# Kernel optimization log

Hardware: AMD Instinct MI355X
Metric: run time of the kernel (lower is better)

The kernel has to match this reference:

```python
import jax, jax.numpy as jnp
import numpy as np

B, N, IN_DIM, D, H = 8, 2048, 256, 512, 4
HD = D // H
GX, GY = 8, 8
IMG_W, IMG_H = 256.0, 256.0
CW, CH = IMG_W / GX, IMG_H / GY
NBH = 1
EPS = 1e-5


def setup_inputs() -> dict:
    key = jax.random.key(0)
    ks = jax.random.split(key, 12)
    s = 0.02
    rn = lambda k, sh: jax.random.normal(k, sh, jnp.float32) * s
    return {
        'features': jax.random.normal(ks[0], (B, N, IN_DIM), jnp.float32),
        'coords': jax.random.uniform(ks[1], (B, N, 2), jnp.float32) * IMG_W,
        'W_feat': rn(ks[2], (IN_DIM, D)), 'b_feat': jnp.zeros((D,), jnp.float32),
        'W_p1': rn(ks[3], (2, D // 2)), 'b_p1': jnp.zeros((D // 2,), jnp.float32),
        'W_p2': rn(ks[4], (D // 2, D)), 'b_p2': jnp.zeros((D,), jnp.float32),
        'Wq': rn(ks[5], (D, D)), 'bq': jnp.zeros((D,), jnp.float32),
        'Wk': rn(ks[6], (D, D)), 'bk': jnp.zeros((D,), jnp.float32),
        'Wv': rn(ks[7], (D, D)), 'bv': jnp.zeros((D,), jnp.float32),
        'Wo': rn(ks[8], (D, D)), 'bo': jnp.zeros((D,), jnp.float32),
        'gamma': jnp.ones((D,), jnp.float32), 'beta': jnp.zeros((D,), jnp.float32),
    }


def reference(features, coords, W_feat, b_feat, W_p1, b_p1, W_p2, b_p2,
              Wq, bq, Wk, bk, Wv, bv, Wo, bo, gamma, beta):
    feat = features @ W_feat + b_feat                          # [B,N,D]
    # --- grid bucketing (mean feature per occupied cell) ---
    gx = jnp.clip((coords[..., 0] / CW).astype(jnp.int32), 0, GX - 1)
    gy = jnp.clip((coords[..., 1] / CH).astype(jnp.int32), 0, GY - 1)
    cell = gx * GY + gy                                        # [B,N]
    G = GX * GY
    seg = (jnp.arange(B, dtype=jnp.int32)[:, None] * G + cell).reshape(-1)
    sums = jax.ops.segment_sum(feat.reshape(B * N, D), seg, num_segments=B * G)
    counts = jax.ops.segment_sum(jnp.ones((B * N,), jnp.float32), seg, num_segments=B * G)
    mean = (sums / jnp.maximum(counts, 1.0)[:, None]).reshape(B, G, D)
    counts = counts.reshape(B, G)
    # --- neighbor cells (static 3x3 window for neighborhood=1) ---
    offs = np.array([(dx, dy) for dx in range(-NBH, NBH + 1) for dy in range(-NBH, NBH + 1)], np.int32)
    K = offs.shape[0]
    pe = jnp.asarray(offs, jnp.float32)
    pe = jax.nn.relu(pe @ W_p1 + b_p1) @ W_p2 + b_p2           # [K,D] pos enc of offsets
    ngx = gx[..., None] + offs[:, 0]                           # [B,N,K]
    ngy = gy[..., None] + offs[:, 1]
    inb = (ngx >= 0) & (ngx < GX) & (ngy >= 0) & (ngy < GY)
    nidx = jnp.clip(ngx, 0, GX - 1) * GY + jnp.clip(ngy, 0, GY - 1)
    bidx = jnp.arange(B)[:, None, None]
    valid = inb & (counts[bidx, nidx] > 0)                     # [B,N,K]
    keys = mean[bidx, nidx] + pe                               # [B,N,K,D]
    # --- per-point attention over <=9 neighbor cells ---
    q = (feat @ Wq + bq).reshape(B, N, H, HD)
    k = (keys @ Wk + bk).reshape(B, N, K, H, HD)
    v = (keys @ Wv + bv).reshape(B, N, K, H, HD)
    scores = jnp.einsum('bnhd,bnkhd->bnhk', q, k) / np.float32(np.sqrt(HD))
    scores = jnp.where(valid[:, :, None, :], scores, jnp.float32(-1e9))
    attn = jax.nn.softmax(scores, axis=-1)
    agg = jnp.einsum('bnhk,bnkhd->bnhd', attn, v).reshape(B, N, D) @ Wo + bo
    enhanced = feat + agg                                      # residual (dropout in eval = identity)
    mu = enhanced.mean(-1, keepdims=True)
    var = enhanced.var(-1, keepdims=True)
    return (enhanced - mu) / jnp.sqrt(var + EPS) * gamma + beta
```

## Files before the change

### kernel.cpp

```cpp
#include <hip/hip_runtime.h>
#include <stdint.h>

typedef unsigned short u16;
typedef unsigned int u32;
typedef __bf16 bf16x8 __attribute__((ext_vector_type(8)));
typedef float f32x4 __attribute__((ext_vector_type(4)));

#define NBATCH 8
#define NPT    2048
#define NPTS   16384
#define INDIM  256
#define DD     512
#define GG     64

__device__ __forceinline__ u16 f2bf(float f){
  u32 u = __builtin_bit_cast(u32, f);
  u += 0x7fffu + ((u >> 16) & 1u);
  return (u16)(u >> 16);
}
__device__ __forceinline__ float bf2f(u16 h){
  u32 u = ((u32)h) << 16;
  return __builtin_bit_cast(float, u);
}
__device__ __forceinline__ void load8(const float* __restrict__ p, float* r){
  float4 a = *(const float4*)p;
  float4 b = *(const float4*)(p + 4);
  r[0]=a.x;r[1]=a.y;r[2]=a.z;r[3]=a.w;r[4]=b.x;r[5]=b.y;r[6]=b.z;r[7]=b.w;
}
__device__ __forceinline__ void load8bf(const u16* __restrict__ p, float* r){
  uint4 v = *(const uint4*)p;
  r[0]=bf2f((u16)v.x); r[1]=bf2f((u16)(v.x>>16));
  r[2]=bf2f((u16)v.y); r[3]=bf2f((u16)(v.y>>16));
  r[4]=bf2f((u16)v.z); r[5]=bf2f((u16)(v.z>>16));
  r[6]=bf2f((u16)v.w); r[7]=bf2f((u16)(v.w>>16));
}
__device__ __forceinline__ void load8bf_lds(const u16* p, float* r){
  uint4 v = *(const uint4*)p;
  r[0]=bf2f((u16)v.x); r[1]=bf2f((u16)(v.x>>16));
  r[2]=bf2f((u16)v.y); r[3]=bf2f((u16)(v.y>>16));
  r[4]=bf2f((u16)v.z); r[5]=bf2f((u16)(v.z>>16));
  r[6]=bf2f((u16)v.w); r[7]=bf2f((u16)(v.w>>16));
}
__device__ __forceinline__ void store8(float* __restrict__ p, const float* r){
  float4 a; a.x=r[0];a.y=r[1];a.z=r[2];a.w=r[3];
  float4 b; b.x=r[4];b.y=r[5];b.z=r[6];b.w=r[7];
  *(float4*)p = a; *(float4*)(p+4) = b;
}
__device__ __forceinline__ uint4 pack8(const float* a){
  uint4 pk;
  pk.x = (u32)f2bf(a[0]) | ((u32)f2bf(a[1]) << 16);
  pk.y = (u32)f2bf(a[2]) | ((u32)f2bf(a[3]) << 16);
  pk.z = (u32)f2bf(a[4]) | ((u32)f2bf(a[5]) << 16);
  pk.w = (u32)f2bf(a[6]) | ((u32)f2bf(a[7]) << 16);
  return pk;
}
typedef __attribute__((address_space(1))) unsigned as1u;
typedef __attribute__((address_space(3))) unsigned as3u;
__device__ __forceinline__ void gload16(const void* g, void* l){
  __builtin_amdgcn_global_load_lds((as1u*)(uintptr_t)g, (as3u*)(uintptr_t)l, 16, 0, 0);
}

__device__ __forceinline__ void transpose64(const float* __restrict__ src, int scols,
                                            u16* __restrict__ dst, int dcols,
                                            int r0, int c0, char* smem, int t){
  float (*sh)[65] = (float(*)[65])smem;
  #pragma unroll
  for (int i = 0; i < 16; i++){
    int idx = i*256 + t;
    int r = idx >> 6, c = idx & 63;
    sh[r][c] = src[(size_t)(r0 + r)*scols + c0 + c];
  }
  __syncthreads();
  #pragma unroll
  for (int i = 0; i < 8; i++){
    int idx = i*512 + t*2;
    int oR = idx >> 6, oC = idx & 63;
    u32 pk = (u32)f2bf(sh[oC][oR]) | ((u32)f2bf(sh[oC+1][oR]) << 16);
    *(u32*)(dst + (size_t)(c0 + oR)*dcols + r0 + oC) = pk;
  }
}

#define P_R1 2048
#define P_R2 2112
#define P_R3 2368
#define P_R4 2400
#define P_R5 2409
#define P_R6 2411
#define P_R7 2415
#define P_NB 2423
__global__ __launch_bounds__(256) void prep_kernel(
    const float* __restrict__ features, const float* __restrict__ W_feat,
    const float* __restrict__ Wq, const float* __restrict__ Wk,
    const float* __restrict__ Wv, const float* __restrict__ Wo,
    const float* __restrict__ W_p1, const float* __restrict__ b_p1,
    const float* __restrict__ W_p2, const float* __restrict__ b_p2,
    const float* __restrict__ b_feat, const float* __restrict__ bq,
    const float* __restrict__ bk, const float* __restrict__ bv,
    const float* __restrict__ coords,
    u16* __restrict__ featA, u16* __restrict__ W_feat_bf,
    u16* __restrict__ WqkvT, u16* __restrict__ WoT, u16* __restrict__ WcatT,
    u16* __restrict__ peD, float* __restrict__ bfq, float* __restrict__ biaskv,
    int* __restrict__ order, int* __restrict__ counts, int* __restrict__ cellstart)
{
  __shared__ __align__(16) char smem[34048];
  int bid = blockIdx.x, t = threadIdx.x;
  if (bid < P_R1){
    int i = bid*256 + t;
    float r[8]; load8(features + (size_t)i*8, r);
    *(uint4*)(featA + (size_t)i*8) = pack8(r);
  } else if (bid < P_R2){
    int i = (bid - P_R1)*256 + t;
    float r[8]; load8(W_feat + (size_t)i*8, r);
    *(uint4*)(W_feat_bf + (size_t)i*8) = pack8(r);
  } else if (bid < P_R3){
    int rel = bid - P_R2;
    int mat = rel >> 6, tile = rel & 63;
    int r0 = (tile >> 3)*64, c0 = (tile & 7)*64;
    const float* src = mat==0 ? Wq : (mat==1 ? Wk : (mat==2 ? Wv : Wo));
    u16* dst = mat==0 ? WqkvT : (mat==1 ? WqkvT + (size_t)512*DD
                     : (mat==2 ? WqkvT + (size_t)1024*DD : WoT));
    transpose64(src, DD, dst, DD, r0, c0, smem, t);
  } else if (bid < P_R4){
    int rel = bid - P_R3;
    int r0 = (rel >> 3)*64, c0 = (rel & 7)*64;
    transpose64(W_feat, DD, WcatT, INDIM, r0, c0, smem, t);
  } else if (bid < P_R5){
    int kk = bid - P_R4;
    float dx = (float)(kk/3 - 1), dy = (float)(kk%3 - 1);
    float* h = (float*)smem;
    float hv = dx*W_p1[t] + dy*W_p1[256 + t] + b_p1[t];
    h[t] = hv > 0.f ? hv : 0.f;
    __syncthreads();
    float acc0 = b_p2[t], acc1 = b_p2[t + 256];
    for (int c = 0; c < 256; c++){
      float hc = h[c];
      acc0 += hc * W_p2[(size_t)c*DD + t];
      acc1 += hc * W_p2[(size_t)c*DD + t + 256];
    }
    peD[(size_t)kk*DD + t]       = f2bf(acc0);
    peD[(size_t)kk*DD + t + 256] = f2bf(acc1);
  } else if (bid < P_R6){
    int i = (bid - P_R5)*256 + t;
    float* bfs = (float*)smem;
    bfs[t] = b_feat[t]; bfs[t + 256] = b_feat[t + 256];
    __syncthreads();
    float acc = 0.f;
    for (int k = 0; k < DD; k++) acc += bfs[k] * Wq[(size_t)k*DD + i];
    bfq[i] = acc + bq[i];
  } else if (bid < P_R7){
    int n = (bid - P_R6)*256 + t;
    float* bfs = (float*)smem;
    bfs[t] = b_feat[t]; bfs[t + 256] = b_feat[t + 256];
    __syncthreads();
    const float* W = (n < 512) ? Wk : Wv;
    int c = n & 511;
    float acc = 0.f;
    for (int k = 0; k < DD; k++) acc += bfs[k] * W[(size_t)k*DD + c];
    biaskv[n] = acc + ((n < 512) ? bk[c] : bv[c]);
  } else {
    int b = bid - P_R7;
    u16 (*hist)[65] = (u16(*)[65])smem;
    int* tot  = (int*)(smem + 33280);
    int* base = (int*)(smem + 33536);
    #pragma unroll
    for (int i = 0; i < 65; i++) hist[t][i] = 0;
    int myc[8];
    float cxy[16];
    load8(coords + (size_t)(b*NPT + t*8)*2,     cxy);
    load8(coords + (size_t)(b*NPT + t*8)*2 + 8, cxy + 8);
    #pragma unroll
    for (int i = 0; i < 8; i++){
      int gx = (int)(cxy[2*i]   * (1.0f/32.0f)); gx = gx < 0 ? 0 : (gx > 7 ? 7 : gx);
      int gy = (int)(cxy[2*i+1] * (1.0f/32.0f)); gy = gy < 0 ? 0 : (gy > 7 ? 7 : gy);
      myc[i] = gx*8 + gy;
      hist[t][myc[i]]++;
    }
    __syncthreads();
    if (t < GG){
      int acc = 0;
      for (int tt = 0; tt < 256; tt++){ int v = hist[tt][t]; hist[tt][t] = (u16)acc; acc += v; }
      tot[t] = acc;
    }
    __syncthreads();
    if (t == 0){
      int acc = 0;
      for (int g = 0; g < GG; g++){ base[g] = acc; acc += tot[g]; }
    }
    __syncthreads();
    if (t < GG){
      counts[b*GG + t] = tot[t];
      cellstart[b*GG + t] = base[t];
    }
    #pragma unroll
    for (int i = 0; i < 8; i++){
      int g = myc[i];
      int local = 0;
      #pragma unroll
      for (int j = 0; j < 8; j++) local += (j < i && myc[j] == g) ? 1 : 0;
      order[b*NPT + base[g] + (int)hist[t][g] + local] = t*8 + i;
    }
  }
}

#define BM 128
#define BN 128
#define GEMM_PIPE(SMEMB, Aptr, Btptr, Kv, GXv, NWGv, UIDX)                         \
  u16* lA_ = (u16*)(SMEMB);                                                        \
  u16* lB_ = (u16*)((char*)(SMEMB) + 16384);                                       \
  int orig_ = (UIDX);                                                              \
  int swz_ = (orig_ & 7)*((NWGv) >> 3) + (orig_ >> 3);                             \
  int m0 = (swz_ / (GXv)) * BM, n0 = (swz_ % (GXv)) * BN;                          \
  int lane = tid & 63;                                                             \
  int wv = tid >> 6;                                                               \
  int wm = (wv >> 1) * 64, wn = (wv & 1) * 64;                                     \
  int lr = lane & 15;                                                              \
  int kg = (lane >> 4) << 3;                                                       \
  f32x4 acc[4][4] = {};                                                            \
  {                                                                                \
    int srow = lane >> 2;                                                          \
    int scol = (lane & 3) << 3;                                                    \
    const u16* gA0 = (Aptr)  + (size_t)(m0 + wv*32 + srow)*(Kv) + scol;            \
    const u16* gB0 = (Btptr) + (size_t)(n0 + wv*32 + srow)*(Kv) + scol;            \
    int lofs = (wv*32)*32;                                                         \
    int steps = (Kv) >> 5;                                                         \
    gload16(gA0,                   lA_ + lofs);                                    \
    gload16(gA0 + (size_t)16*(Kv), lA_ + lofs + 512);                              \
    gload16(gB0,                   lB_ + lofs);                                    \
    gload16(gB0 + (size_t)16*(Kv), lB_ + lofs + 512);                              \
    __syncthreads();                                                               \
    for (int s = 0; s < steps; s++){                                               \
      int cur = s & 1;                                                             \
      u16* lAc = lA_ + cur*4096;                                                   \
      u16* lBc = lB_ + cur*4096;                                                   \
      if (s + 1 < steps){                                                          \
        int kt = (s + 1) << 5;                                                     \
        u16* lAn = lA_ + (cur^1)*4096;                                             \
        u16* lBn = lB_ + (cur^1)*4096;                                             \
        gload16(gA0 + kt,                   lAn + lofs);                           \
        gload16(gA0 + kt + (size_t)16*(Kv), lAn + lofs + 512);                     \
        gload16(gB0 + kt,                   lBn + lofs);                           \
        gload16(gB0 + kt + (size_t)16*(Kv), lBn + lofs + 512);                     \
      }                                                                            \
      bf16x8 af[4], bfv[4];                                                        \
      _Pragma("unroll")                                                            \
      for (int i = 0; i < 4; i++) af[i]  = *(const bf16x8*)&lAc[(wm + i*16 + lr)*32 + kg]; \
      _Pragma("unroll")                                                            \
      for (int j = 0; j < 4; j++) bfv[j] = *(const bf16x8*)&lBc[(wn + j*16 + lr)*32 + kg]; \
      _Pragma("unroll")                                                            \
      for (int i = 0; i < 4; i++)                                                  \
        _Pragma("unroll")                                                          \
        for (int j = 0; j < 4; j++)                                                \
          acc[i][j] = __builtin_amdgcn_mfma_f32_16x16x32_bf16(af[i], bfv[j], acc[i][j], 0, 0, 0); \
      __syncthreads();                                                             \
    }                                                                              \
  }                                                                                \
  int lrow = (lane >> 4) << 2;

#define EPI_BF16(SMEMB, DST, LDN, BIAS)                                            \
  {                                                                                \
    u16* Cs = (u16*)(SMEMB);                                                       \
    _Pragma("unroll")                                                              \
    for (int j = 0; j < 4; j++){                                                   \
      int col = wn + j*16 + lr;                                                    \
      float bcol = (BIAS)[n0 + col];                                               \
      _Pragma("unroll")                                                            \
      for (int i = 0; i < 4; i++){                                                 \
        int r0 = wm + i*16 + lrow;                                                 \
        _Pragma("unroll")                                                          \
        for (int r = 0; r < 4; r++)                                                \
          Cs[(r0 + r)*136 + col] = f2bf(acc[i][j][r] + bcol);                      \
      }                                                                            \
    }                                                                              \
    __syncthreads();                                                               \
    _Pragma("unroll")                                                              \
    for (int k = 0; k < 8; k++){                                                   \
      int idx = k*256 + tid;                                                       \
      int row = idx >> 4, c8 = (idx & 15) << 3;                                    \
      *(uint4*)&(DST)[(size_t)(m0 + row)*(LDN) + n0 + c8] = *(uint4*)&Cs[row*136 + c8]; \
    }                                                                              \
  }

__global__ __launch_bounds__(256) void mid_kernel(
    const u16* __restrict__ WqkvT, const u16* __restrict__ W_feat_bf,
    const u16* __restrict__ peD, u16* __restrict__ Xout, float* __restrict__ meanKV,
    const u16* __restrict__ featA, const int* __restrict__ order,
    const int* __restrict__ counts, const int* __restrict__ cellstart,
    u16* __restrict__ meanF, const u16* __restrict__ WcatT,
    const float* __restrict__ b_feat, u16* __restrict__ feat_bf)
{
  __shared__ __align__(16) char SMEM[34816];
  int tid = threadIdx.x;
  if (blockIdx.x < 24){
    GEMM_PIPE(SMEM, WqkvT, W_feat_bf, 512, 2, 24, (int)blockIdx.x)
    #pragma unroll
    for (int j = 0; j < 4; j++){
      int col = n0 + wn + j*16 + lr;
      #pragma unroll
      for (int i = 0; i < 4; i++){
        int row0 = m0 + wm + i*16 + lrow;
        #pragma unroll
        for (int r = 0; r < 4; r++)
          Xout[(size_t)(row0 + r)*INDIM + col] = f2bf(acc[i][j][r]);
      }
    }
  } else if (blockIdx.x < 60){
    float* pesh = (float*)SMEM;
    int bid2 = blockIdx.x - 24;
    int kk = bid2 >> 2, seg = bid2 & 3;
    int n = seg*256 + tid;
    pesh[tid]       = bf2f(peD[(size_t)kk*DD + tid]);
    pesh[tid + 256] = bf2f(peD[(size_t)kk*DD + tid + 256]);
    __syncthreads();
    const u16* wrow = WqkvT + (size_t)(512 + n)*DD;
    float acc = 0.f;
    for (int d8 = 0; d8 < 64; d8++){
      float w8[8]; load8bf(wrow + d8*8, w8);
      #pragma unroll
      for (int j = 0; j < 8; j++) acc += pesh[d8*8 + j]*w8[j];
    }
    meanKV[(size_t)(512 + kk)*1024 + n] = acc;
  } else if (blockIdx.x < 572){
    float (*part)[2] = (float(*)[2])SMEM;
    int bg = blockIdx.x - 60;
    int b = bg >> 6;
    int p = tid & 127, half = tid >> 7;
    int cnt = counts[bg], start = cellstart[bg];
    const int* ord = order + b*NPT + start;
    float a0 = 0.f, a1 = 0.f;
    for (int n = half; n < cnt; n += 2){
      u32 v = *(const u32*)(featA + (((size_t)(b*NPT + ord[n])) << 8) + p*2);
      a0 += bf2f((u16)v); a1 += bf2f((u16)(v >> 16));
    }
    if (half){ part[p][0] = a0; part[p][1] = a1; }
    __syncthreads();
    if (!half){
      a0 += part[p][0]; a1 += part[p][1];
      float inv = 1.f / (float)(cnt > 0 ? cnt : 1);
      *(u32*)(meanF + (size_t)bg*INDIM + p*2) =
          (u32)f2bf(a0*inv) | ((u32)f2bf(a1*inv) << 16);
    }
  } else {
    GEMM_PIPE(SMEM, featA, WcatT, 256, 4, 512, (int)blockIdx.x - 572)
    EPI_BF16(SMEM, feat_bf, DD, b_feat)
  }
}

__global__ __launch_bounds__(256) void qmean_kernel(
    const u16* __restrict__ featA, const u16* __restrict__ WfqT,
    const u16* __restrict__ meanF, const u16* __restrict__ WfkvT,
    const float* __restrict__ bfq, const float* __restrict__ biaskv,
    u16* __restrict__ q_bf, float* __restrict__ meanKV)
{
  __shared__ __align__(16) char SMEM[34816];
  int tid = threadIdx.x;
  if (blockIdx.x < 512){
    GEMM_PIPE(SMEM, featA, WfqT, 256, 4, 512, (int)blockIdx.x)
    EPI_BF16(SMEM, q_bf, DD, bfq)
  } else {
    GEMM_PIPE(SMEM, meanF, WfkvT, 256, 8, 32, (int)blockIdx.x - 512)
    #pragma unroll
    for (int j = 0; j < 4; j++){
      int col = n0 + wn + j*16 + lr;
      float bcol = biaskv[col];
      #pragma unroll
      for (int i = 0; i < 4; i++){
        int row0 = m0 + wm + i*16 + lrow;
        #pragma unroll
        for (int r = 0; r < 4; r++)
          meanKV[(size_t)(row0 + r)*1024 + col] = acc[i][j][r] + bcol;
      }
    }
  }
}

__global__ __launch_bounds__(1024) void attn_cells(
    const u16* __restrict__ q, const float* __restrict__ meanKV,
    const int* __restrict__ order, const int* __restrict__ counts,
    const int* __restrict__ cellstart, u16* __restrict__ agg)
{
  int bg = blockIdx.x;
  int b = bg >> 6, c = bg & 63;
  int gx = c >> 3, gy = c & 7;
  __shared__ __align__(16) u16 Kf[9][DD];
  __shared__ __align__(16) u16 Vf[9][DD];
  __shared__ int vrow[9];
  int t = threadIdx.x;
  if (t < 9){
    int dx = t/3 - 1, dy = t%3 - 1;
    int nx = gx + dx, ny = gy + dy;
    int inb = ((unsigned)nx < 8u) && ((unsigned)ny < 8u);
    int row = b*GG + (((nx&7) << 3) | (ny&7));
    vrow[t] = (inb && counts[row] > 0) ? row : -1;
  }
  __syncthreads();
  int d = 2*(t & 255);
  for (int kk = (t >> 8); kk < 9; kk += 4){
    int row = vrow[kk];
    if (row >= 0){
      float2 mk = *(const float2*)&meanKV[(size_t)row*1024 + d];
      float2 pk = *(const float2*)&meanKV[(size_t)(512+kk)*1024 + d];
      float2 mv = *(const float2*)&meanKV[(size_t)row*1024 + 512 + d];
      float2 pv = *(const float2*)&meanKV[(size_t)(512+kk)*1024 + 512 + d];
      *(u32*)&Kf[kk][d] = (u32)f2bf(mk.x+pk.x) | ((u32)f2bf(mk.y+pk.y) << 16);
      *(u32*)&Vf[kk][d] = (u32)f2bf(mv.x+pv.x) | ((u32)f2bf(mv.y+pv.y) << 16);
    }
  }
  __syncthreads();
  int cnt = counts[bg];
  int wv = t >> 6, lane = t & 63;
  const int* ord = order + b*NPT + cellstart[bg];
  for (int i = wv; i < cnt; i += 16){
    size_t p = (size_t)b*NPT + ord[i];
    float qv[8];
    load8bf(q + p*DD + lane*8, qv);
    float s[9];
    #pragma unroll
    for (int kk = 0; kk < 9; kk++){
      float partial = 0.f;
      if (vrow[kk] >= 0){
        float kv[8]; load8bf(&Kf[kk][lane*8], kv);
        #pragma unroll
        for (int j = 0; j < 8; j++) partial += qv[j]*kv[j];
      }
      partial += __shfl_xor(partial, 1);
      partial += __shfl_xor(partial, 2);
      partial += __shfl_xor(partial, 4);
      partial += __shfl_xor(partial, 8);
      s[kk] = (vrow[kk] >= 0) ? partial * 0.08838834764831843f : -1e30f;
    }
    float mx = s[0];
    #pragma unroll
    for (int kk = 1; kk < 9; kk++) mx = fmaxf(mx, s[kk]);
    float w[9], sum = 0.f;
    #pragma unroll
    for (int kk = 0; kk < 9; kk++){
      w[kk] = (vrow[kk] >= 0) ? __expf(s[kk] - mx) : 0.f;
      sum += w[kk];
    }
    float inv = 1.f / sum;
    float a[8] = {0,0,0,0,0,0,0,0};
    #pragma unroll
    for (int kk = 0; kk < 9; kk++){
      if (vrow[kk] >= 0){
        float wk = w[kk] * inv;
        float vv[8]; load8bf(&Vf[kk][lane*8], vv);
        #pragma unroll
        for (int j = 0; j < 8; j++) a[j] += wk*vv[j];
      }
    }
    *(uint4*)&agg[p*DD + lane*8] = pack8(a);
  }
}

__global__ __launch_bounds__(512) void linln_kernel(
    const u16* __restrict__ agg_bf, const u16* __restrict__ WoT,
    const float* __restrict__ bo, const u16* __restrict__ feat_bf,
    const float* __restrict__ gamma, const float* __restrict__ beta,
    float* __restrict__ out)
{
  __shared__ __align__(16) char SMEM[73728];
  u16* lA = (u16*)SMEM;
  u16* lB = (u16*)(SMEM + 8192);
  int tid = threadIdx.x;
  int lane = tid & 63;
  int wvv = tid >> 6;
  int m0 = blockIdx.x * 64;
  int wm2 = (wvv >> 2) * 32;
  int wn2 = (wvv & 3) * 128;
  int lr = lane & 15;
  int kg = (lane >> 4) << 3;
  int srow = lane >> 2;
  int scol = (lane & 3) << 3;
  f32x4 acc[2][8] = {};
  {
    const u16* gB0 = WoT + (size_t)(wvv*64 + srow)*DD + scol;
    int lBoff = (wvv*64)*32;
    const u16* gA0 = agg_bf + (size_t)(m0 + (wvv&3)*16 + srow)*DD + scol;
    int lAoff = ((wvv&3)*16)*32;
    bool doA = (wvv < 4);
    #pragma unroll
    for (int c = 0; c < 4; c++)
      gload16(gB0 + (size_t)(c*16)*DD, lB + lBoff + c*16*32);
    if (doA) gload16(gA0, lA + lAoff);
    __syncthreads();
    for (int s = 0; s < 16; s++){
      int cur = s & 1;
      u16* lAc = lA + cur*2048;
      u16* lBc = lB + cur*16384;
      if (s + 1 < 16){
        int kt = (s + 1) << 5;
        u16* lAn = lA + (cur^1)*2048;
        u16* lBn = lB + (cur^1)*16384;
        #pragma unroll
        for (int c = 0; c < 4; c++)
          gload16(gB0 + kt + (size_t)(c*16)*DD, lBn + lBoff + c*16*32);
        if (doA) gload16(gA0 + kt, lAn + lAoff);
      }
      bf16x8 af[2], bfv[8];
      #pragma unroll
      for (int i = 0; i < 2; i++) af[i]  = *(const bf16x8*)&lAc[(wm2 + i*16 + lr)*32 + kg];
      #pragma unroll
      for (int j = 0; j < 8; j++) bfv[j] = *(const bf16x8*)&lBc[(wn2 + j*16 + lr)*32 + kg];
      #pragma unroll
      for (int i = 0; i < 2; i++)
        #pragma unroll
        for (int j = 0; j < 8; j++)
          acc[i][j] = __builtin_amdgcn_mfma_f32_16x16x32_bf16(af[i], bfv[j], acc[i][j], 0, 0, 0);
      __syncthreads();
    }
  }
  int lrow = (lane >> 4) << 2;
  u16* Cs = (u16*)SMEM;
  #pragma unroll
  for (int j = 0; j < 8; j++){
    int col = wn2 + j*16 + lr;
    float bcol = bo[col];
    #pragma unroll
    for (int i = 0; i < 2; i++){
      int r0 = wm2 + i*16 + lrow;
      #pragma unroll
      for (int r = 0; r < 4; r++)
        Cs[(r0 + r)*520 + col] = f2bf(acc[i][j][r] + bcol);
    }
  }
  __syncthreads();
  float gv[8], bev[8];
  load8(gamma + lane*8, gv);
  load8(beta + lane*8, bev);
  for (int rr = 0; rr < 8; rr++){
    int row = wvv*8 + rr;
    float lv[8], fv[8];
    load8bf_lds(&Cs[row*520 + lane*8], lv);
    load8bf(feat_bf + (size_t)(m0 + row)*DD + lane*8, fv);
    float e[8], s1 = 0.f, s2 = 0.f;
    #pragma unroll
    for (int j = 0; j < 8; j++){ e[j] = fv[j] + lv[j]; s1 += e[j]; s2 += e[j]*e[j]; }
    #pragma unroll
    for (int m = 1; m < 64; m <<= 1){ s1 += __shfl_xor(s1, m); s2 += __shfl_xor(s2, m); }
    float mu  = s1 * (1.f/512.f);
    float var = s2 * (1.f/512.f) - mu*mu;
    float istd = rsqrtf(var + 1e-5f);
    float o[8];
    #pragma unroll
    for (int j = 0; j < 8; j++) o[j] = (e[j] - mu)*istd*gv[j] + bev[j];
    store8(out + (size_t)(m0 + row)*DD + lane*8, o);
  }
}

extern "C" void kernel_launch(void* const* d_in, const int* in_sizes, int n_in,
                              void* d_out, int out_size, void* d_ws, size_t ws_size,
                              hipStream_t stream) {
  (void)in_sizes; (void)n_in; (void)out_size; (void)ws_size;
  const float* features = (const float*)d_in[0];
  const float* coords   = (const float*)d_in[1];
  const float* W_feat   = (const float*)d_in[2];
  const float* b_feat   = (const float*)d_in[3];
  const float* W_p1     = (const float*)d_in[4];
  const float* b_p1     = (const float*)d_in[5];
  const float* W_p2     = (const float*)d_in[6];
  const float* b_p2     = (const float*)d_in[7];
  const float* Wq = (const float*)d_in[8];  const float* bq = (const float*)d_in[9];
  const float* Wk = (const float*)d_in[10]; const float* bk = (const float*)d_in[11];
  const float* Wv = (const float*)d_in[12]; const float* bv = (const float*)d_in[13];
  const float* Wo = (const float*)d_in[14]; const float* bo = (const float*)d_in[15];
  const float* gamma = (const float*)d_in[16]; const float* beta = (const float*)d_in[17];
  float* out = (float*)d_out;

  char* ws = (char*)d_ws;
  size_t off = 0;
  auto alloc = [&](size_t bytes) -> void* {
    void* p = ws + off;
    off = (off + bytes + 255) & ~(size_t)255;
    return p;
  };
  u16*   featA     = (u16*)  alloc((size_t)NPTS*INDIM*2);
  u16*   feat_bf   = (u16*)  alloc((size_t)NPTS*DD*2);
  u16*   q_bf      = (u16*)  alloc((size_t)NPTS*DD*2);
  u16*   agg_bf    = (u16*)  alloc((size_t)NPTS*DD*2);
  u16*   W_feat_bf = (u16*)  alloc((size_t)INDIM*DD*2);
  u16*   WqkvT     = (u16*)  alloc((size_t)1536*DD*2);
  u16*   WoT       = (u16*)  alloc((size_t)DD*DD*2);
  u16*   WcatT     = (u16*)  alloc((size_t)512*INDIM*2);
  u16*   Xout      = (u16*)  alloc((size_t)1536*INDIM*2);
  u16*   peD       = (u16*)  alloc((size_t)9*DD*2);
  u16*   meanF     = (u16*)  alloc((size_t)512*INDIM*2);
  float* meanKV    = (float*)alloc((size_t)640*1024*4);
  float* bfq       = (float*)alloc((size_t)DD*4);
  float* biaskv    = (float*)alloc((size_t)1024*4);
  int*   order     = (int*)  alloc((size_t)NPTS*4);
  int*   counts    = (int*)  alloc((size_t)NBATCH*GG*4);
  int*   cellstart = (int*)  alloc((size_t)NBATCH*GG*4);
  u16*   WfqT      = Xout;
  u16*   WfkvT     = Xout + (size_t)512*INDIM;

  prep_kernel<<<P_NB, 256, 0, stream>>>(
      features, W_feat, Wq, Wk, Wv, Wo, W_p1, b_p1, W_p2, b_p2,
      b_feat, bq, bk, bv, coords,
      featA, W_feat_bf, WqkvT, WoT, WcatT, peD, bfq, biaskv,
      order, counts, cellstart);
  mid_kernel<<<1084, 256, 0, stream>>>(
      WqkvT, W_feat_bf, peD, Xout, meanKV, featA, order, counts, cellstart,
      meanF, WcatT, b_feat, feat_bf);
  qmean_kernel<<<544, 256, 0, stream>>>(
      featA, WfqT, meanF, WfkvT, bfq, biaskv, q_bf, meanKV);
  attn_cells<<<NBATCH*GG, 1024, 0, stream>>>(q_bf, meanKV, order, counts, cellstart, agg_bf);
  linln_kernel<<<NPTS/64, 512, 0, stream>>>(agg_bf, WoT, bo, feat_bf, gamma, beta, out);
}
```

Before: 101.8 us.

## Merge mid and qmean kernels, move weight-product GEMM into prep

The W_fkvq = Wqkv·W_feat product is now computed inside prep_kernel, by extra blocks that read fp32 weights directly and convert them to bf16 on the fly. This removes the separate W_feat bf16 conversion. The feat and q projections become one GEMM over the concatenated [W_feat^T; WfqT] buffer, which relies on WcatT and Xout sitting next to each other in the workspace. The per-cell mean K/V projection is fused into the segment-mean blocks as a matvec, so mid_kernel and qmean_kernel collapse into one launch. This drops one kernel boundary and an intermediate buffer. The trade-off is an unpipelined GEMM tail in prep and a slower scalar matvec in place of the MFMA mean GEMM.

New measurement: 219.6 us. 116% more time.

```diff
diff --git a/kernel.cpp b/kernel.cpp
--- a/kernel.cpp
+++ b/kernel.cpp
@@ -81,13 +81,13 @@
 }
 
 #define P_R1 2048
-#define P_R2 2112
-#define P_R3 2368
-#define P_R4 2400
-#define P_R5 2409
-#define P_R6 2411
-#define P_R7 2415
-#define P_NB 2423
+#define P_R2 2304
+#define P_R3 2336
+#define P_R4 2345
+#define P_R5 2347
+#define P_R6 2351
+#define P_R7 2359
+#define P_NB 2383
 __global__ __launch_bounds__(256) void prep_kernel(
     const float* __restrict__ features, const float* __restrict__ W_feat,
     const float* __restrict__ Wq, const float* __restrict__ Wk,
@@ -97,8 +97,9 @@
     const float* __restrict__ b_feat, const float* __restrict__ bq,
     const float* __restrict__ bk, const float* __restrict__ bv,
     const float* __restrict__ coords,
-    u16* __restrict__ featA, u16* __restrict__ W_feat_bf,
+    u16* __restrict__ featA,
     u16* __restrict__ WqkvT, u16* __restrict__ WoT, u16* __restrict__ WcatT,
+    u16* __restrict__ Xout,
     u16* __restrict__ peD, float* __restrict__ bfq, float* __restrict__ biaskv,
     int* __restrict__ order, int* __restrict__ counts, int* __restrict__ cellstart)
 {
@@ -109,23 +110,19 @@
     float r[8]; load8(features + (size_t)i*8, r);
     *(uint4*)(featA + (size_t)i*8) = pack8(r);
   } else if (bid < P_R2){
-    int i = (bid - P_R1)*256 + t;
-    float r[8]; load8(W_feat + (size_t)i*8, r);
-    *(uint4*)(W_feat_bf + (size_t)i*8) = pack8(r);
-  } else if (bid < P_R3){
-    int rel = bid - P_R2;
+    int rel = bid - P_R1;
     int mat = rel >> 6, tile = rel & 63;
     int r0 = (tile >> 3)*64, c0 = (tile & 7)*64;
     const float* src = mat==0 ? Wq : (mat==1 ? Wk : (mat==2 ? Wv : Wo));
     u16* dst = mat==0 ? WqkvT : (mat==1 ? WqkvT + (size_t)512*DD
                      : (mat==2 ? WqkvT + (size_t)1024*DD : WoT));
     transpose64(src, DD, dst, DD, r0, c0, smem, t);
-  } else if (bid < P_R4){
-    int rel = bid - P_R3;
+  } else if (bid < P_R3){
+    int rel = bid - P_R2;
     int r0 = (rel >> 3)*64, c0 = (rel & 7)*64;
     transpose64(W_feat, DD, WcatT, INDIM, r0, c0, smem, t);
-  } else if (bid < P_R5){
-    int kk = bid - P_R4;
+  } else if (bid < P_R4){
+    int kk = bid - P_R3;
     float dx = (float)(kk/3 - 1), dy = (float)(kk%3 - 1);
     float* h = (float*)smem;
     float hv = dx*W_p1[t] + dy*W_p1[256 + t] + b_p1[t];
@@ -139,16 +136,16 @@
     }
     peD[(size_t)kk*DD + t]       = f2bf(acc0);
     peD[(size_t)kk*DD + t + 256] = f2bf(acc1);
-  } else if (bid < P_R6){
-    int i = (bid - P_R5)*256 + t;
+  } else if (bid < P_R5){
+    int i = (bid - P_R4)*256 + t;
     float* bfs = (float*)smem;
     bfs[t] = b_feat[t]; bfs[t + 256] = b_feat[t + 256];
     __syncthreads();
     float acc = 0.f;
     for (int k = 0; k < DD; k++) acc += bfs[k] * Wq[(size_t)k*DD + i];
     bfq[i] = acc + bq[i];
-  } else if (bid < P_R7){
-    int n = (bid - P_R6)*256 + t;
+  } else if (bid < P_R6){
+    int n = (bid - P_R5)*256 + t;
     float* bfs = (float*)smem;
     bfs[t] = b_feat[t]; bfs[t + 256] = b_feat[t + 256];
     __syncthreads();
@@ -157,8 +154,8 @@
     float acc = 0.f;
     for (int k = 0; k < DD; k++) acc += bfs[k] * W[(size_t)k*DD + c];
     biaskv[n] = acc + ((n < 512) ? bk[c] : bv[c]);
-  } else {
-    int b = bid - P_R7;
+  } else if (bid < P_R7){
+    int b = bid - P_R6;
     u16 (*hist)[65] = (u16(*)[65])smem;
     int* tot  = (int*)(smem + 33280);
     int* base = (int*)(smem + 33536);
@@ -198,6 +195,63 @@
       #pragma unroll
       for (int j = 0; j < 8; j++) local += (j < i && myc[j] == g) ? 1 : 0;
       order[b*NPT + base[g] + (int)hist[t][g] + local] = t*8 + i;
+    }
+  } else {
+    int u = bid - P_R7;
+    int m0 = (u >> 1) * 128;
+    int n0 = (u & 1) * 128;
+    const float* Wm = (m0 < 512) ? Wq : (m0 < 1024 ? Wk : Wv);
+    int nw0 = m0 & 511;
+    u16* lA = (u16*)smem;
+    u16* lB = (u16*)(smem + 10240);
+    int lane = t & 63, wv2 = t >> 6;
+    int wm = (wv2 >> 1)*64, wn = (wv2 & 1)*64;
+    int lr = lane & 15, kg = (lane >> 4) << 3;
+    f32x4 acc[4][4] = {};
+    for (int kt = 0; kt < 512; kt += 32){
+      #pragma unroll
+      for (int i = 0; i < 4; i++){
+        int idx = i*256 + t;
+        int rd = idx & 31;
+        int c4 = idx >> 5;
+        float4 v = *(const float4*)&Wm[(size_t)(kt + rd)*DD + nw0 + c4*4];
+        lA[(c4*4+0)*40 + rd] = f2bf(v.x);
+        lA[(c4*4+1)*40 + rd] = f2bf(v.y);
+        lA[(c4*4+2)*40 + rd] = f2bf(v.z);
+        lA[(c4*4+3)*40 + rd] = f2bf(v.w);
+      }
+      #pragma unroll
+      for (int i = 0; i < 4; i++){
+        int idx = i*256 + t;
+        int row = idx >> 3, c4 = idx & 7;
+        float4 v = *(const float4*)&W_feat[(size_t)(n0 + row)*DD + kt + c4*4];
+        u16* dst = &lB[row*40 + c4*4];
+        dst[0]=f2bf(v.x); dst[1]=f2bf(v.y); dst[2]=f2bf(v.z); dst[3]=f2bf(v.w);
+      }
+      __syncthreads();
+      bf16x8 af[4], bfv[4];
+      #pragma unroll
+      for (int i = 0; i < 4; i++) af[i]  = *(const bf16x8*)&lA[(wm + i*16 + lr)*40 + kg];
+      #pragma unroll
+      for (int j = 0; j < 4; j++) bfv[j] = *(const bf16x8*)&lB[(wn + j*16 + lr)*40 + kg];
+      #pragma unroll
+      for (int i = 0; i < 4; i++)
+        #pragma unroll
+        for (int j = 0; j < 4; j++)
+          acc[i][j] = __builtin_amdgcn_mfma_f32_16x16x32_bf16(af[i], bfv[j], acc[i][j], 0, 0, 0);
+      __syncthreads();
+    }
+    int lrow = (lane >> 4) << 2;
+    #pragma unroll
+    for (int j = 0; j < 4; j++){
+      int col = n0 + wn + j*16 + lr;
+      #pragma unroll
+      for (int i = 0; i < 4; i++){
+        int row0 = m0 + wm + i*16 + lrow;
+        #pragma unroll
+        for (int r = 0; r < 4; r++)
+          Xout[(size_t)(row0 + r)*INDIM + col] = f2bf(acc[i][j][r]);
+      }
     }
   }
 }
@@ -256,72 +310,48 @@
   }                                                                                \
   int lrow = (lane >> 4) << 2;
 
-#define EPI_BF16(SMEMB, DST, LDN, BIAS)                                            \
-  {                                                                                \
-    u16* Cs = (u16*)(SMEMB);                                                       \
-    _Pragma("unroll")                                                              \
-    for (int j = 0; j < 4; j++){                                                   \
-      int col = wn + j*16 + lr;                                                    \
-      float bcol = (BIAS)[n0 + col];                                               \
-      _Pragma("unroll")                                                            \
-      for (int i = 0; i < 4; i++){                                                 \
-        int r0 = wm + i*16 + lrow;                                                 \
-        _Pragma("unroll")                                                          \
-        for (int r = 0; r < 4; r++)                                                \
-          Cs[(r0 + r)*136 + col] = f2bf(acc[i][j][r] + bcol);                      \
-      }                                                                            \
-    }                                                                              \
-    __syncthreads();                                                               \
-    _Pragma("unroll")                                                              \
-    for (int k = 0; k < 8; k++){                                                   \
-      int idx = k*256 + tid;                                                       \
-      int row = idx >> 4, c8 = (idx & 15) << 3;                                    \
-      *(uint4*)&(DST)[(size_t)(m0 + row)*(LDN) + n0 + c8] = *(uint4*)&Cs[row*136 + c8]; \
-    }                                                                              \
-  }
-
-__global__ __launch_bounds__(256) void mid_kernel(
-    const u16* __restrict__ WqkvT, const u16* __restrict__ W_feat_bf,
-    const u16* __restrict__ peD, u16* __restrict__ Xout, float* __restrict__ meanKV,
-    const u16* __restrict__ featA, const int* __restrict__ order,
-    const int* __restrict__ counts, const int* __restrict__ cellstart,
-    u16* __restrict__ meanF, const u16* __restrict__ WcatT,
-    const float* __restrict__ b_feat, u16* __restrict__ feat_bf)
+__global__ __launch_bounds__(256) void big2_kernel(
+    const u16* __restrict__ featA, const u16* __restrict__ WcatT,
+    const u16* __restrict__ WfkvT, const u16* __restrict__ WqkvT,
+    const u16* __restrict__ peD,
+    const float* __restrict__ b_feat, const float* __restrict__ bfq,
+    const float* __restrict__ biaskv,
+    const int* __restrict__ order, const int* __restrict__ counts,
+    const int* __restrict__ cellstart,
+    u16* __restrict__ feat_bf, u16* __restrict__ q_bf, float* __restrict__ meanKV)
 {
   __shared__ __align__(16) char SMEM[34816];
   int tid = threadIdx.x;
-  if (blockIdx.x < 24){
-    GEMM_PIPE(SMEM, WqkvT, W_feat_bf, 512, 2, 24, (int)blockIdx.x)
+  if (blockIdx.x < 1024){
+    GEMM_PIPE(SMEM, featA, WcatT, 256, 8, 1024, (int)blockIdx.x)
+    int half = n0 >> 9;
+    u16* outp = half ? q_bf : feat_bf;
+    const float* bias = half ? bfq : b_feat;
+    int nb = n0 & 511;
+    u16* Cs = (u16*)SMEM;
     #pragma unroll
     for (int j = 0; j < 4; j++){
-      int col = n0 + wn + j*16 + lr;
+      int col = wn + j*16 + lr;
+      float bcol = bias[nb + col];
       #pragma unroll
       for (int i = 0; i < 4; i++){
-        int row0 = m0 + wm + i*16 + lrow;
+        int r0 = wm + i*16 + lrow;
         #pragma unroll
         for (int r = 0; r < 4; r++)
-          Xout[(size_t)(row0 + r)*INDIM + col] = f2bf(acc[i][j][r]);
-      }
-    }
-  } else if (blockIdx.x < 60){
-    float* pesh = (float*)SMEM;
-    int bid2 = blockIdx.x - 24;
-    int kk = bid2 >> 2, seg = bid2 & 3;
-    int n = seg*256 + tid;
-    pesh[tid]       = bf2f(peD[(size_t)kk*DD + tid]);
-    pesh[tid + 256] = bf2f(peD[(size_t)kk*DD + tid + 256]);
-    __syncthreads();
-    const u16* wrow = WqkvT + (size_t)(512 + n)*DD;
-    float acc = 0.f;
-    for (int d8 = 0; d8 < 64; d8++){
-      float w8[8]; load8bf(wrow + d8*8, w8);
-      #pragma unroll
-      for (int j = 0; j < 8; j++) acc += pesh[d8*8 + j]*w8[j];
-    }
-    meanKV[(size_t)(512 + kk)*1024 + n] = acc;
-  } else if (blockIdx.x < 572){
+          Cs[(r0 + r)*136 + col] = f2bf(acc[i][j][r] + bcol);
+      }
+    }
+    __syncthreads();
+    #pragma unroll
+    for (int k = 0; k < 8; k++){
+      int idx = k*256 + tid;
+      int row = idx >> 4, c8 = (idx & 15) << 3;
+      *(uint4*)&outp[(size_t)(m0 + row)*DD + nb + c8] = *(uint4*)&Cs[row*136 + c8];
+    }
+  } else if (blockIdx.x < 1536){
     float (*part)[2] = (float(*)[2])SMEM;
-    int bg = blockIdx.x - 60;
+    float* mf = (float*)(SMEM + 1024);
+    int bg = blockIdx.x - 1024;
     int b = bg >> 6;
     int p = tid & 127, half = tid >> 7;
     int cnt = counts[bg], start = cellstart[bg];
@@ -336,40 +366,38 @@
     if (!half){
       a0 += part[p][0]; a1 += part[p][1];
       float inv = 1.f / (float)(cnt > 0 ? cnt : 1);
-      *(u32*)(meanF + (size_t)bg*INDIM + p*2) =
-          (u32)f2bf(a0*inv) | ((u32)f2bf(a1*inv) << 16);
+      mf[2*p]   = bf2f(f2bf(a0*inv));
+      mf[2*p+1] = bf2f(f2bf(a1*inv));
+    }
+    __syncthreads();
+    #pragma unroll
+    for (int cc = 0; cc < 4; cc++){
+      int c = cc*256 + tid;
+      const u16* wrow = WfkvT + (size_t)c*INDIM;
+      float acc = 0.f;
+      for (int k8 = 0; k8 < 32; k8++){
+        float w8[8]; load8bf(wrow + k8*8, w8);
+        #pragma unroll
+        for (int j = 0; j < 8; j++) acc += mf[k8*8 + j]*w8[j];
+      }
+      meanKV[(size_t)bg*1024 + c] = acc + biaskv[c];
     }
   } else {
-    GEMM_PIPE(SMEM, featA, WcatT, 256, 4, 512, (int)blockIdx.x - 572)
-    EPI_BF16(SMEM, feat_bf, DD, b_feat)
-  }
-}
-
-__global__ __launch_bounds__(256) void qmean_kernel(
-    const u16* __restrict__ featA, const u16* __restrict__ WfqT,
-    const u16* __restrict__ meanF, const u16* __restrict__ WfkvT,
-    const float* __restrict__ bfq, const float* __restrict__ biaskv,
-    u16* __restrict__ q_bf, float* __restrict__ meanKV)
-{
-  __shared__ __align__(16) char SMEM[34816];
-  int tid = threadIdx.x;
-  if (blockIdx.x < 512){
-    GEMM_PIPE(SMEM, featA, WfqT, 256, 4, 512, (int)blockIdx.x)
-    EPI_BF16(SMEM, q_bf, DD, bfq)
-  } else {
-    GEMM_PIPE(SMEM, meanF, WfkvT, 256, 8, 32, (int)blockIdx.x - 512)
-    #pragma unroll
-    for (int j = 0; j < 4; j++){
-      int col = n0 + wn + j*16 + lr;
-      float bcol = biaskv[col];
-      #pragma unroll
-      for (int i = 0; i < 4; i++){
-        int row0 = m0 + wm + i*16 + lrow;
-        #pragma unroll
-        for (int r = 0; r < 4; r++)
-          meanKV[(size_t)(row0 + r)*1024 + col] = acc[i][j][r] + bcol;
-      }
-    }
+    float* pesh = (float*)SMEM;
+    int bid2 = blockIdx.x - 1536;
+    int kk = bid2 >> 2, seg = bid2 & 3;
+    int n = seg*256 + tid;
+    pesh[tid]       = bf2f(peD[(size_t)kk*DD + tid]);
+    pesh[tid + 256] = bf2f(peD[(size_t)kk*DD + tid + 256]);
+    __syncthreads();
+    const u16* wrow = WqkvT + (size_t)(512 + n)*DD;
+    float acc = 0.f;
+    for (int d8 = 0; d8 < 64; d8++){
+      float w8[8]; load8bf(wrow + d8*8, w8);
+      #pragma unroll
+      for (int j = 0; j < 8; j++) acc += pesh[d8*8 + j]*w8[j];
+    }
+    meanKV[(size_t)(512 + kk)*1024 + n] = acc;
   }
 }
 
@@ -577,32 +605,27 @@
   u16*   feat_bf   = (u16*)  alloc((size_t)NPTS*DD*2);
   u16*   q_bf      = (u16*)  alloc((size_t)NPTS*DD*2);
   u16*   agg_bf    = (u16*)  alloc((size_t)NPTS*DD*2);
-  u16*   W_feat_bf = (u16*)  alloc((size_t)INDIM*DD*2);
   u16*   WqkvT     = (u16*)  alloc((size_t)1536*DD*2);
   u16*   WoT       = (u16*)  alloc((size_t)DD*DD*2);
   u16*   WcatT     = (u16*)  alloc((size_t)512*INDIM*2);
   u16*   Xout      = (u16*)  alloc((size_t)1536*INDIM*2);
   u16*   peD       = (u16*)  alloc((size_t)9*DD*2);
-  u16*   meanF     = (u16*)  alloc((size_t)512*INDIM*2);
   float* meanKV    = (float*)alloc((size_t)640*1024*4);
   float* bfq       = (float*)alloc((size_t)DD*4);
   float* biaskv    = (float*)alloc((size_t)1024*4);
   int*   order     = (int*)  alloc((size_t)NPTS*4);
   int*   counts    = (int*)  alloc((size_t)NBATCH*GG*4);
   int*   cellstart = (int*)  alloc((size_t)NBATCH*GG*4);
-  u16*   WfqT      = Xout;
   u16*   WfkvT     = Xout + (size_t)512*INDIM;
 
   prep_kernel<<<P_NB, 256, 0, stream>>>(
       features, W_feat, Wq, Wk, Wv, Wo, W_p1, b_p1, W_p2, b_p2,
       b_feat, bq, bk, bv, coords,
-      featA, W_feat_bf, WqkvT, WoT, WcatT, peD, bfq, biaskv,
+      featA, WqkvT, WoT, WcatT, Xout, peD, bfq, biaskv,
       order, counts, cellstart);
-  mid_kernel<<<1084, 256, 0, stream>>>(
-      WqkvT, W_feat_bf, peD, Xout, meanKV, featA, order, counts, cellstart,
-      meanF, WcatT, b_feat, feat_bf);
-  qmean_kernel<<<544, 256, 0, stream>>>(
-      featA, WfqT, meanF, WfkvT, bfq, biaskv, q_bf, meanKV);
+  big2_kernel<<<1572, 256, 0, stream>>>(
+      featA, WcatT, WfkvT, WqkvT, peD, b_feat, bfq, biaskv,
+      order, counts, cellstart, feat_bf, q_bf, meanKV);
   attn_cells<<<NBATCH*GG, 1024, 0, stream>>>(q_bf, meanKV, order, counts, cellstart, agg_bf);
   linln_kernel<<<NPTS/64, 512, 0, stream>>>(agg_bf, WoT, bo, feat_bf, gamma, beta, out);
 }
```
